# Kernel tuning notes

Measured on AMD Instinct MI355X. Metric: run time of the kernel, lower is better.

The kernel has to match this reference:

```python
import jax, jax.numpy as jnp
import numpy as np

B, N, D, K, H = 32768, 17, 2, 3, 64


def _mlp_params(key, n, d_in, d_hid, d_out):
    k1, k2, k3, k4 = jax.random.split(key, 4)
    W1 = jax.random.normal(k1, (n, d_in, d_hid), jnp.float32) / np.sqrt(d_in)
    b1 = jnp.zeros((n, d_hid), jnp.float32)
    W2 = jax.random.normal(k2, (n, d_hid, d_out), jnp.float32) / np.sqrt(d_hid)
    b2 = jnp.zeros((n, d_out), jnp.float32)
    return W1, b1, W2, b2


def setup_inputs() -> dict:
    key = jax.random.key(0)
    kp, kk, kw, kb = jax.random.split(key, 4)
    pred_pts = jax.random.normal(kp, (B, N, D), jnp.float32)
    kW1, kb1, kW2, kb2 = _mlp_params(kk, N, D, H, K)            # k_nets
    wW1, wb1, wW2, wb2 = _mlp_params(kw, N, D, H, K)            # weight_nets
    bW1, bb1, bW2, bb2 = _mlp_params(kb, N, D, 2 * H, K * 2 * D)  # basis_nets
    return dict(pred_pts=pred_pts,
                kW1=kW1, kb1=kb1, kW2=kW2, kb2=kb2,
                wW1=wW1, wb1=wb1, wW2=wW2, wb2=wb2,
                bW1=bW1, bb1=bb1, bW2=bW2, bb2=bb2)


def _per_joint_mlp(x, W1, b1, W2, b2):
    # x: [B,N,D]; W1: [N,D,Hd]; W2: [N,Hd,O]
    h = jax.nn.relu(jnp.einsum('bnd,ndh->bnh', x, W1) + b1[None])
    return jnp.einsum('bnh,nho->bno', h, W2) + b2[None]


def reference(pred_pts, kW1, kb1, kW2, kb2, wW1, wb1, wW2, wb2, bW1, bb1, bW2, bb2):
    Bc, Nc, Dc = pred_pts.shape
    Kc = kW2.shape[-1]

    # k-selection head (eval mode: argmax, +1)
    k_logits = _per_joint_mlp(pred_pts, kW1, kb1, kW2, kb2)      # [B,N,K]
    k_js = jnp.argmax(k_logits, axis=-1) + 1                     # [B,N] int

    # mixture weights
    w = jax.nn.softmax(_per_joint_mlp(pred_pts, wW1, wb1, wW2, wb2), axis=-1)  # [B,N,K]

    # basis parameters: mu, sigma = exp(log_sigma)
    params = _per_joint_mlp(pred_pts, bW1, bb1, bW2, bb2).reshape(Bc, Nc, Kc, 2 * Dc)
    mu = params[..., :Dc]                                         # [B,N,K,D]
    sigma = jnp.exp(params[..., Dc:])                             # [B,N,K,D]

    # top-k selection by descending weight (indices are constants w.r.t. grad)
    idx = jnp.argsort(-w, axis=-1)                                # [B,N,K]
    mu_top = jnp.take_along_axis(mu, idx[..., None], axis=2)      # [B,N,K,D]
    sigma_top = jnp.take_along_axis(sigma, idx[..., None], axis=2)
    mask = jnp.arange(Kc)[None, None, :] < k_js[..., None]        # [B,N,K] bool

    # pack float outputs: weights + selected (mu, sigma) -> [B,N,K,1+2D]
    out = jnp.concatenate([w[..., None], mu_top, sigma_top], axis=-1)
    return out, k_js, mask
```

## Files before the change

### kernel.cpp

```cpp
#include <hip/hip_runtime.h>
#include <cmath>

#define NBATCH 32768
#define NJOINT 17
#define OUT0_ELEMS (NBATCH * NJOINT * 15)
#define KJS_OFF    OUT0_ELEMS
#define MASK_OFF   (KJS_OFF + NBATCH * NJOINT)

__device__ __forceinline__ float sel3f(int i, float a, float b, float c) {
    return (i == 0) ? a : ((i == 1) ? b : c);
}

__global__ __launch_bounds__(256) void mdn_fused(
    const float* __restrict__ pred_pts,
    const float* __restrict__ kW1, const float* __restrict__ kb1,
    const float* __restrict__ kW2, const float* __restrict__ kb2,
    const float* __restrict__ wW1, const float* __restrict__ wb1,
    const float* __restrict__ wW2, const float* __restrict__ wb2,
    const float* __restrict__ bW1, const float* __restrict__ bb1,
    const float* __restrict__ bW2, const float* __restrict__ bb2,
    float* __restrict__ out)
{
    const int n = blockIdx.y;
    const int b = blockIdx.x * 256 + threadIdx.x;
    const int p = b * NJOINT + n;

    const float2 xv = *reinterpret_cast<const float2*>(pred_pts + 2 * p);
    const float x0f = xv.x, x1f = xv.y;
    const double x0 = (double)x0f, x1 = (double)x1f;

    double kl0, kl1, kl2;
    {
        const float* W1a = kW1 + n * 128;
        const float* W1b = W1a + 64;
        const float* b1  = kb1 + n * 64;
        const float* W2  = kW2 + n * 192;
        kl0 = (double)kb2[n * 3 + 0];
        kl1 = (double)kb2[n * 3 + 1];
        kl2 = (double)kb2[n * 3 + 2];
        #pragma unroll 8
        for (int h = 0; h < 64; ++h) {
            double hv = fma(x1, (double)W1b[h], fma(x0, (double)W1a[h], (double)b1[h]));
            hv = fmax(hv, 0.0);
            kl0 = fma(hv, (double)W2[h * 3 + 0], kl0);
            kl1 = fma(hv, (double)W2[h * 3 + 1], kl1);
            kl2 = fma(hv, (double)W2[h * 3 + 2], kl2);
        }
    }
    int kj = 0;
    {
        double m = kl0;
        if (kl1 > m) { m = kl1; kj = 1; }
        if (kl2 > m) { kj = 2; }
    }

    double wl0, wl1, wl2;
    {
        const float* W1a = wW1 + n * 128;
        const float* W1b = W1a + 64;
        const float* b1  = wb1 + n * 64;
        const float* W2  = wW2 + n * 192;
        wl0 = (double)wb2[n * 3 + 0];
        wl1 = (double)wb2[n * 3 + 1];
        wl2 = (double)wb2[n * 3 + 2];
        #pragma unroll 8
        for (int h = 0; h < 64; ++h) {
            double hv = fma(x1, (double)W1b[h], fma(x0, (double)W1a[h], (double)b1[h]));
            hv = fmax(hv, 0.0);
            wl0 = fma(hv, (double)W2[h * 3 + 0], wl0);
            wl1 = fma(hv, (double)W2[h * 3 + 1], wl1);
            wl2 = fma(hv, (double)W2[h * 3 + 2], wl2);
        }
    }
    int i0 = 0;
    {
        double m = wl0;
        if (wl1 > m) { m = wl1; i0 = 1; }
        if (wl2 > m) { i0 = 2; }
    }
    const int ia = (i0 == 0) ? 1 : 0;
    const int ib = (i0 == 2) ? 1 : 2;
    const double wa = ia ? wl1 : wl0;
    const double wb = (ib == 1) ? wl1 : wl2;
    const int i1 = (wb > wa) ? ib : ia;
    const int i2 = (wb > wa) ? ia : ib;

    const double mw = fmax(fmax(wl0, wl1), wl2);
    const float e0 = __expf((float)(wl0 - mw));
    const float e1 = __expf((float)(wl1 - mw));
    const float e2 = __expf((float)(wl2 - mw));
    const float inv = 1.0f / (e0 + e1 + e2);
    const float p0 = e0 * inv, p1 = e1 * inv, p2 = e2 * inv;

    float acc[12];
    {
        const float* W1a = bW1 + n * 256;
        const float* W1b = W1a + 128;
        const float* b1  = bb1 + n * 128;
        const float* W2  = bW2 + n * 1536;
        const float* b2  = bb2 + n * 12;
        #pragma unroll
        for (int j = 0; j < 12; ++j) acc[j] = b2[j];
        #pragma unroll 4
        for (int h = 0; h < 128; ++h) {
            float hv = fmaxf(fmaf(x1f, W1b[h], fmaf(x0f, W1a[h], b1[h])), 0.0f);
            #pragma unroll
            for (int j = 0; j < 12; ++j)
                acc[j] = fmaf(hv, W2[h * 12 + j], acc[j]);
        }
    }

    float r[15];
    r[0]  = p0; r[5] = p1; r[10] = p2;

    r[1]  = sel3f(i0, acc[0], acc[4], acc[8]);
    r[2]  = sel3f(i0, acc[1], acc[5], acc[9]);
    r[3]  = __expf(sel3f(i0, acc[2], acc[6], acc[10]));
    r[4]  = __expf(sel3f(i0, acc[3], acc[7], acc[11]));

    r[6]  = sel3f(i1, acc[0], acc[4], acc[8]);
    r[7]  = sel3f(i1, acc[1], acc[5], acc[9]);
    r[8]  = __expf(sel3f(i1, acc[2], acc[6], acc[10]));
    r[9]  = __expf(sel3f(i1, acc[3], acc[7], acc[11]));

    r[11] = sel3f(i2, acc[0], acc[4], acc[8]);
    r[12] = sel3f(i2, acc[1], acc[5], acc[9]);
    r[13] = __expf(sel3f(i2, acc[2], acc[6], acc[10]));
    r[14] = __expf(sel3f(i2, acc[3], acc[7], acc[11]));

    float* o = out + (size_t)p * 15;
    #pragma unroll
    for (int i = 0; i < 15; ++i) o[i] = r[i];

    out[KJS_OFF + p] = (float)(kj + 1);

    float* mk = out + MASK_OFF + (size_t)p * 3;
    mk[0] = 1.0f;
    mk[1] = (kj >= 1) ? 1.0f : 0.0f;
    mk[2] = (kj >= 2) ? 1.0f : 0.0f;
}

extern "C" void kernel_launch(void* const* d_in, const int* in_sizes, int n_in,
                              void* d_out, int out_size, void* d_ws, size_t ws_size,
                              hipStream_t stream) {
    (void)in_sizes; (void)n_in; (void)d_ws; (void)ws_size; (void)out_size;
    dim3 grid(NBATCH / 256, NJOINT);
    mdn_fused<<<grid, 256, 0, stream>>>(
        (const float*)d_in[0],
        (const float*)d_in[1], (const float*)d_in[2],
        (const float*)d_in[3], (const float*)d_in[4],
        (const float*)d_in[5], (const float*)d_in[6],
        (const float*)d_in[7], (const float*)d_in[8],
        (const float*)d_in[9], (const float*)d_in[10],
        (const float*)d_in[11], (const float*)d_in[12],
        (float*)d_out);
}
```

Baseline: 146.6 us.

## Compute small MLP heads in packed fp32 with fp64 fallback near ties

```diff
diff --git a/kernel.cpp b/kernel.cpp
--- a/kernel.cpp
+++ b/kernel.cpp
@@ -7,8 +7,56 @@
 #define KJS_OFF    OUT0_ELEMS
 #define MASK_OFF   (KJS_OFF + NBATCH * NJOINT)
 
+typedef float v2f __attribute__((ext_vector_type(2)));
+
+__device__ __forceinline__ v2f pkfma(v2f a, v2f b, v2f c) { return __builtin_elementwise_fma(a, b, c); }
+__device__ __forceinline__ v2f pkmax(v2f a, v2f b)        { return __builtin_elementwise_max(a, b); }
+
 __device__ __forceinline__ float sel3f(int i, float a, float b, float c) {
     return (i == 0) ? a : ((i == 1) ? b : c);
+}
+
+__device__ __noinline__ void mlp64_small(
+    const float* __restrict__ W1a, const float* __restrict__ W1b,
+    const float* __restrict__ b1,  const float* __restrict__ W2,
+    const float* __restrict__ b2,
+    double x0, double x1, double& l0, double& l1, double& l2)
+{
+    l0 = (double)b2[0]; l1 = (double)b2[1]; l2 = (double)b2[2];
+    for (int h = 0; h < 64; ++h) {
+        double hv = fma(x1, (double)W1b[h], fma(x0, (double)W1a[h], (double)b1[h]));
+        hv = fmax(hv, 0.0);
+        l0 = fma(hv, (double)W2[h * 3 + 0], l0);
+        l1 = fma(hv, (double)W2[h * 3 + 1], l1);
+        l2 = fma(hv, (double)W2[h * 3 + 2], l2);
+    }
+}
+
+__device__ __forceinline__ void mlp32_small(
+    const float* __restrict__ W1a, const float* __restrict__ W1b,
+    const float* __restrict__ b1,  const float* __restrict__ W2,
+    const float* __restrict__ b2,
+    v2f vx0, v2f vx1, float& l0, float& l1, float& l2)
+{
+    v2f a0 = {0.f, 0.f}, a1 = {0.f, 0.f}, a2 = {0.f, 0.f};
+    const v2f vzero = {0.f, 0.f};
+    #pragma unroll 8
+    for (int h = 0; h < 64; h += 2) {
+        const v2f w1a = *reinterpret_cast<const v2f*>(W1a + h);
+        const v2f w1b = *reinterpret_cast<const v2f*>(W1b + h);
+        const v2f bb  = *reinterpret_cast<const v2f*>(b1 + h);
+        const v2f hv  = pkmax(pkfma(vx1, w1b, pkfma(vx0, w1a, bb)), vzero);
+        v2f w20, w21, w22;
+        w20.x = W2[h * 3 + 0]; w20.y = W2[h * 3 + 3];
+        w21.x = W2[h * 3 + 1]; w21.y = W2[h * 3 + 4];
+        w22.x = W2[h * 3 + 2]; w22.y = W2[h * 3 + 5];
+        a0 = pkfma(hv, w20, a0);
+        a1 = pkfma(hv, w21, a1);
+        a2 = pkfma(hv, w22, a2);
+    }
+    l0 = a0.x + a0.y + b2[0];
+    l1 = a1.x + a1.y + b2[1];
+    l2 = a2.x + a2.y + b2[2];
 }
 
 __global__ __launch_bounds__(256) void mdn_fused(
@@ -27,25 +75,21 @@
 
     const float2 xv = *reinterpret_cast<const float2*>(pred_pts + 2 * p);
     const float x0f = xv.x, x1f = xv.y;
-    const double x0 = (double)x0f, x1 = (double)x1f;
-
-    double kl0, kl1, kl2;
-    {
-        const float* W1a = kW1 + n * 128;
-        const float* W1b = W1a + 64;
-        const float* b1  = kb1 + n * 64;
-        const float* W2  = kW2 + n * 192;
-        kl0 = (double)kb2[n * 3 + 0];
-        kl1 = (double)kb2[n * 3 + 1];
-        kl2 = (double)kb2[n * 3 + 2];
-        #pragma unroll 8
-        for (int h = 0; h < 64; ++h) {
-            double hv = fma(x1, (double)W1b[h], fma(x0, (double)W1a[h], (double)b1[h]));
-            hv = fmax(hv, 0.0);
-            kl0 = fma(hv, (double)W2[h * 3 + 0], kl0);
-            kl1 = fma(hv, (double)W2[h * 3 + 1], kl1);
-            kl2 = fma(hv, (double)W2[h * 3 + 2], kl2);
-        }
+    const v2f vx0 = {x0f, x0f}, vx1 = {x1f, x1f};
+
+    const float* kW1a = kW1 + n * 128;
+    const float* kW1b = kW1a + 64;
+    const float* kb1p = kb1 + n * 64;
+    const float* kW2p = kW2 + n * 192;
+    const float* kb2p = kb2 + n * 3;
+    float kf0, kf1, kf2;
+    mlp32_small(kW1a, kW1b, kb1p, kW2p, kb2p, vx0, vx1, kf0, kf1, kf2);
+    double kl0 = (double)kf0, kl1 = (double)kf1, kl2 = (double)kf2;
+    {
+        const float d01 = fabsf(kf0 - kf1), d02 = fabsf(kf0 - kf2), d12 = fabsf(kf1 - kf2);
+        const float sc = fmaxf(fmaxf(fabsf(kf0), fabsf(kf1)), fabsf(kf2));
+        if (fminf(fminf(d01, d02), d12) < 1e-4f * fmaxf(sc, 1.0f))
+            mlp64_small(kW1a, kW1b, kb1p, kW2p, kb2p, (double)x0f, (double)x1f, kl0, kl1, kl2);
     }
     int kj = 0;
     {
@@ -54,23 +98,19 @@
         if (kl2 > m) { kj = 2; }
     }
 
-    double wl0, wl1, wl2;
-    {
-        const float* W1a = wW1 + n * 128;
-        const float* W1b = W1a + 64;
-        const float* b1  = wb1 + n * 64;
-        const float* W2  = wW2 + n * 192;
-        wl0 = (double)wb2[n * 3 + 0];
-        wl1 = (double)wb2[n * 3 + 1];
-        wl2 = (double)wb2[n * 3 + 2];
-        #pragma unroll 8
-        for (int h = 0; h < 64; ++h) {
-            double hv = fma(x1, (double)W1b[h], fma(x0, (double)W1a[h], (double)b1[h]));
-            hv = fmax(hv, 0.0);
-            wl0 = fma(hv, (double)W2[h * 3 + 0], wl0);
-            wl1 = fma(hv, (double)W2[h * 3 + 1], wl1);
-            wl2 = fma(hv, (double)W2[h * 3 + 2], wl2);
-        }
+    const float* wW1a = wW1 + n * 128;
+    const float* wW1b = wW1a + 64;
+    const float* wb1p = wb1 + n * 64;
+    const float* wW2p = wW2 + n * 192;
+    const float* wb2p = wb2 + n * 3;
+    float wf0, wf1, wf2;
+    mlp32_small(wW1a, wW1b, wb1p, wW2p, wb2p, vx0, vx1, wf0, wf1, wf2);
+    double wl0 = (double)wf0, wl1 = (double)wf1, wl2 = (double)wf2;
+    {
+        const float d01 = fabsf(wf0 - wf1), d02 = fabsf(wf0 - wf2), d12 = fabsf(wf1 - wf2);
+        const float sc = fmaxf(fmaxf(fabsf(wf0), fabsf(wf1)), fabsf(wf2));
+        if (fminf(fminf(d01, d02), d12) < 1e-4f * fmaxf(sc, 1.0f))
+            mlp64_small(wW1a, wW1b, wb1p, wW2p, wb2p, (double)x0f, (double)x1f, wl0, wl1, wl2);
     }
     int i0 = 0;
     {
@@ -85,14 +125,14 @@
     const int i1 = (wb > wa) ? ib : ia;
     const int i2 = (wb > wa) ? ia : ib;
 
-    const double mw = fmax(fmax(wl0, wl1), wl2);
-    const float e0 = __expf((float)(wl0 - mw));
-    const float e1 = __expf((float)(wl1 - mw));
-    const float e2 = __expf((float)(wl2 - mw));
+    const float mw = fmaxf(fmaxf(wf0, wf1), wf2);
+    const float e0 = __expf(wf0 - mw);
+    const float e1 = __expf(wf1 - mw);
+    const float e2 = __expf(wf2 - mw);
     const float inv = 1.0f / (e0 + e1 + e2);
     const float p0 = e0 * inv, p1 = e1 * inv, p2 = e2 * inv;
 
-    float acc[12];
+    v2f acc[6];
     {
         const float* W1a = bW1 + n * 256;
         const float* W1b = W1a + 128;
@@ -100,33 +140,47 @@
         const float* W2  = bW2 + n * 1536;
         const float* b2  = bb2 + n * 12;
         #pragma unroll
-        for (int j = 0; j < 12; ++j) acc[j] = b2[j];
+        for (int j = 0; j < 6; ++j) acc[j] = *reinterpret_cast<const v2f*>(b2 + 2 * j);
+        const v2f vzero = {0.f, 0.f};
         #pragma unroll 4
-        for (int h = 0; h < 128; ++h) {
-            float hv = fmaxf(fmaf(x1f, W1b[h], fmaf(x0f, W1a[h], b1[h])), 0.0f);
+        for (int h = 0; h < 128; h += 2) {
+            const v2f w1a = *reinterpret_cast<const v2f*>(W1a + h);
+            const v2f w1b = *reinterpret_cast<const v2f*>(W1b + h);
+            const v2f bb  = *reinterpret_cast<const v2f*>(b1 + h);
+            const v2f hv2 = pkmax(pkfma(vx1, w1b, pkfma(vx0, w1a, bb)), vzero);
+            const v2f vhx = {hv2.x, hv2.x};
+            const v2f vhy = {hv2.y, hv2.y};
+            const float* r0 = W2 + h * 12;
             #pragma unroll
-            for (int j = 0; j < 12; ++j)
-                acc[j] = fmaf(hv, W2[h * 12 + j], acc[j]);
+            for (int j = 0; j < 6; ++j)
+                acc[j] = pkfma(vhx, *reinterpret_cast<const v2f*>(r0 + 2 * j), acc[j]);
+            const float* r1 = r0 + 12;
+            #pragma unroll
+            for (int j = 0; j < 6; ++j)
+                acc[j] = pkfma(vhy, *reinterpret_cast<const v2f*>(r1 + 2 * j), acc[j]);
         }
     }
+    float af[12];
+    #pragma unroll
+    for (int j = 0; j < 6; ++j) { af[2 * j] = acc[j].x; af[2 * j + 1] = acc[j].y; }
 
     float r[15];
     r[0]  = p0; r[5] = p1; r[10] = p2;
 
-    r[1]  = sel3f(i0, acc[0], acc[4], acc[8]);
-    r[2]  = sel3f(i0, acc[1], acc[5], acc[9]);
-    r[3]  = __expf(sel3f(i0, acc[2], acc[6], acc[10]));
-    r[4]  = __expf(sel3f(i0, acc[3], acc[7], acc[11]));
-
-    r[6]  = sel3f(i1, acc[0], acc[4], acc[8]);
-    r[7]  = sel3f(i1, acc[1], acc[5], acc[9]);
-    r[8]  = __expf(sel3f(i1, acc[2], acc[6], acc[10]));
-    r[9]  = __expf(sel3f(i1, acc[3], acc[7], acc[11]));
-
-    r[11] = sel3f(i2, acc[0], acc[4], acc[8]);
-    r[12] = sel3f(i2, acc[1], acc[5], acc[9]);
-    r[13] = __expf(sel3f(i2, acc[2], acc[6], acc[10]));
-    r[14] = __expf(sel3f(i2, acc[3], acc[7], acc[11]));
+    r[1]  = sel3f(i0, af[0], af[4], af[8]);
+    r[2]  = sel3f(i0, af[1], af[5], af[9]);
+    r[3]  = __expf(sel3f(i0, af[2], af[6], af[10]));
+    r[4]  = __expf(sel3f(i0, af[3], af[7], af[11]));
+
+    r[6]  = sel3f(i1, af[0], af[4], af[8]);
+    r[7]  = sel3f(i1, af[1], af[5], af[9]);
+    r[8]  = __expf(sel3f(i1, af[2], af[6], af[10]));
+    r[9]  = __expf(sel3f(i1, af[3], af[7], af[11]));
+
+    r[11] = sel3f(i2, af[0], af[4], af[8]);
+    r[12] = sel3f(i2, af[1], af[5], af[9]);
+    r[13] = __expf(sel3f(i2, af[2], af[6], af[10]));
+    r[14] = __expf(sel3f(i2, af[3], af[7], af[11]));
 
     float* o = out + (size_t)p * 15;
     #pragma unroll
```

After: 179.3 us. 1.22x slower.

## Compute k/weight MLPs in fp32 with fp64 fallback for near-ties

Applied to the files above, without the earlier changes.

```diff
diff --git a/kernel.cpp b/kernel.cpp
--- a/kernel.cpp
+++ b/kernel.cpp
@@ -9,6 +9,22 @@
 
 __device__ __forceinline__ float sel3f(int i, float a, float b, float c) {
     return (i == 0) ? a : ((i == 1) ? b : c);
+}
+
+__device__ __noinline__ void mlp64_small(
+    const float* __restrict__ W1a, const float* __restrict__ W1b,
+    const float* __restrict__ b1,  const float* __restrict__ W2,
+    const float* __restrict__ b2,
+    double x0, double x1, double& l0, double& l1, double& l2)
+{
+    l0 = (double)b2[0]; l1 = (double)b2[1]; l2 = (double)b2[2];
+    for (int h = 0; h < 64; ++h) {
+        double hv = fma(x1, (double)W1b[h], fma(x0, (double)W1a[h], (double)b1[h]));
+        hv = fmax(hv, 0.0);
+        l0 = fma(hv, (double)W2[h * 3 + 0], l0);
+        l1 = fma(hv, (double)W2[h * 3 + 1], l1);
+        l2 = fma(hv, (double)W2[h * 3 + 2], l2);
+    }
 }
 
 __global__ __launch_bounds__(256) void mdn_fused(
@@ -27,25 +43,37 @@
 
     const float2 xv = *reinterpret_cast<const float2*>(pred_pts + 2 * p);
     const float x0f = xv.x, x1f = xv.y;
-    const double x0 = (double)x0f, x1 = (double)x1f;
 
-    double kl0, kl1, kl2;
+    const float* kW1a = kW1 + n * 128;
+    const float* kW1b = kW1a + 64;
+    const float* kb1p = kb1 + n * 64;
+    const float* kW2p = kW2 + n * 192;
+    const float* wW1a = wW1 + n * 128;
+    const float* wW1b = wW1a + 64;
+    const float* wb1p = wb1 + n * 64;
+    const float* wW2p = wW2 + n * 192;
+
+    float kf0 = kb2[n * 3 + 0], kf1 = kb2[n * 3 + 1], kf2 = kb2[n * 3 + 2];
+    float wf0 = wb2[n * 3 + 0], wf1 = wb2[n * 3 + 1], wf2 = wb2[n * 3 + 2];
+    #pragma unroll 8
+    for (int h = 0; h < 64; ++h) {
+        const float khv = fmaxf(fmaf(x1f, kW1b[h], fmaf(x0f, kW1a[h], kb1p[h])), 0.0f);
+        kf0 = fmaf(khv, kW2p[h * 3 + 0], kf0);
+        kf1 = fmaf(khv, kW2p[h * 3 + 1], kf1);
+        kf2 = fmaf(khv, kW2p[h * 3 + 2], kf2);
+        const float whv = fmaxf(fmaf(x1f, wW1b[h], fmaf(x0f, wW1a[h], wb1p[h])), 0.0f);
+        wf0 = fmaf(whv, wW2p[h * 3 + 0], wf0);
+        wf1 = fmaf(whv, wW2p[h * 3 + 1], wf1);
+        wf2 = fmaf(whv, wW2p[h * 3 + 2], wf2);
+    }
+
+    double kl0 = (double)kf0, kl1 = (double)kf1, kl2 = (double)kf2;
     {
-        const float* W1a = kW1 + n * 128;
-        const float* W1b = W1a + 64;
-        const float* b1  = kb1 + n * 64;
-        const float* W2  = kW2 + n * 192;
-        kl0 = (double)kb2[n * 3 + 0];
-        kl1 = (double)kb2[n * 3 + 1];
-        kl2 = (double)kb2[n * 3 + 2];
-        #pragma unroll 8
-        for (int h = 0; h < 64; ++h) {
-            double hv = fma(x1, (double)W1b[h], fma(x0, (double)W1a[h], (double)b1[h]));
-            hv = fmax(hv, 0.0);
-            kl0 = fma(hv, (double)W2[h * 3 + 0], kl0);
-            kl1 = fma(hv, (double)W2[h * 3 + 1], kl1);
-            kl2 = fma(hv, (double)W2[h * 3 + 2], kl2);
-        }
+        const float d01 = fabsf(kf0 - kf1), d02 = fabsf(kf0 - kf2), d12 = fabsf(kf1 - kf2);
+        const float sc = fmaxf(fmaxf(fabsf(kf0), fabsf(kf1)), fabsf(kf2));
+        if (fminf(fminf(d01, d02), d12) < 1e-4f * fmaxf(sc, 1.0f))
+            mlp64_small(kW1a, kW1b, kb1p, kW2p, kb2 + n * 3,
+                        (double)x0f, (double)x1f, kl0, kl1, kl2);
     }
     int kj = 0;
     {
@@ -54,23 +82,13 @@
         if (kl2 > m) { kj = 2; }
     }
 
-    double wl0, wl1, wl2;
+    double wl0 = (double)wf0, wl1 = (double)wf1, wl2 = (double)wf2;
     {
-        const float* W1a = wW1 + n * 128;
-        const float* W1b = W1a + 64;
-        const float* b1  = wb1 + n * 64;
-        const float* W2  = wW2 + n * 192;
-        wl0 = (double)wb2[n * 3 + 0];
-        wl1 = (double)wb2[n * 3 + 1];
-        wl2 = (double)wb2[n * 3 + 2];
-        #pragma unroll 8
-        for (int h = 0; h < 64; ++h) {
-            double hv = fma(x1, (double)W1b[h], fma(x0, (double)W1a[h], (double)b1[h]));
-            hv = fmax(hv, 0.0);
-            wl0 = fma(hv, (double)W2[h * 3 + 0], wl0);
-            wl1 = fma(hv, (double)W2[h * 3 + 1], wl1);
-            wl2 = fma(hv, (double)W2[h * 3 + 2], wl2);
-        }
+        const float d01 = fabsf(wf0 - wf1), d02 = fabsf(wf0 - wf2), d12 = fabsf(wf1 - wf2);
+        const float sc = fmaxf(fmaxf(fabsf(wf0), fabsf(wf1)), fabsf(wf2));
+        if (fminf(fminf(d01, d02), d12) < 1e-4f * fmaxf(sc, 1.0f))
+            mlp64_small(wW1a, wW1b, wb1p, wW2p, wb2 + n * 3,
+                        (double)x0f, (double)x1f, wl0, wl1, wl2);
     }
     int i0 = 0;
     {
@@ -85,10 +103,10 @@
     const int i1 = (wb > wa) ? ib : ia;
     const int i2 = (wb > wa) ? ia : ib;
 
-    const double mw = fmax(fmax(wl0, wl1), wl2);
-    const float e0 = __expf((float)(wl0 - mw));
-    const float e1 = __expf((float)(wl1 - mw));
-    const float e2 = __expf((float)(wl2 - mw));
+    const float mw = fmaxf(fmaxf(wf0, wf1), wf2);
+    const float e0 = __expf(wf0 - mw);
+    const float e1 = __expf(wf1 - mw);
+    const float e2 = __expf(wf2 - mw);
     const float inv = 1.0f / (e0 + e1 + e2);
     const float p0 = e0 * inv, p1 = e1 * inv, p2 = e2 * inv;
 
@@ -103,7 +121,7 @@
         for (int j = 0; j < 12; ++j) acc[j] = b2[j];
         #pragma unroll 4
         for (int h = 0; h < 128; ++h) {
-            float hv = fmaxf(fmaf(x1f, W1b[h], fmaf(x0f, W1a[h], b1[h])), 0.0f);
+            const float hv = fmaxf(fmaf(x1f, W1b[h], fmaf(x0f, W1a[h], b1[h])), 0.0f);
             #pragma unroll
             for (int j = 0; j < 12; ++j)
                 acc[j] = fmaf(hv, W2[h * 12 + j], acc[j]);
@@ -112,17 +130,14 @@
 
     float r[15];
     r[0]  = p0; r[5] = p1; r[10] = p2;
-
     r[1]  = sel3f(i0, acc[0], acc[4], acc[8]);
     r[2]  = sel3f(i0, acc[1], acc[5], acc[9]);
     r[3]  = __expf(sel3f(i0, acc[2], acc[6], acc[10]));
     r[4]  = __expf(sel3f(i0, acc[3], acc[7], acc[11]));
-
     r[6]  = sel3f(i1, acc[0], acc[4], acc[8]);
     r[7]  = sel3f(i1, acc[1], acc[5], acc[9]);
     r[8]  = __expf(sel3f(i1, acc[2], acc[6], acc[10]));
     r[9]  = __expf(sel3f(i1, acc[3], acc[7], acc[11]));
-
     r[11] = sel3f(i2, acc[0], acc[4], acc[8]);
     r[12] = sel3f(i2, acc[1], acc[5], acc[9]);
     r[13] = __expf(sel3f(i2, acc[2], acc[6], acc[10]));
```

New measurement: 179.7 us. 1.23x slower.
